# Performance work log

Hardware: AMD Instinct MI355X
Metric: run time of the kernel (lower is better)

Reference implementation:

```python
import jax, jax.numpy as jnp
import numpy as np

H = 128
STEPS = 4
EPS = 1e-5

def _mlp(x, W0, b0, W1, b1, W2, b2):
    x = jax.nn.relu(x @ W0 + b0)
    x = jax.nn.relu(x @ W1 + b1)
    return x @ W2 + b2

def _ln(x, g, b):
    mu = jnp.mean(x, axis=-1, keepdims=True)
    var = jnp.mean((x - mu) ** 2, axis=-1, keepdims=True)
    return (x - mu) * jax.lax.rsqrt(var + EPS) * g + b

def _scores(x, pos):
    # soft assignment of points to graph nodes: softmax over -squared distance
    d2 = (jnp.sum(x * x, -1, keepdims=True)
          - 2.0 * jnp.einsum('bnd,md->bnm', x, pos)
          + jnp.sum(pos * pos, -1))  # [B, Npts, Nnodes]
    return jax.nn.softmax(-d2, axis=-1)

def _block(nodes, senders, receivers, msg_W, msg_b, ln1_g, ln1_b, node_W, node_b, ln2_g, ln2_b):
    # gather edge endpoints, message MLP, layernorm
    m = jnp.concatenate((nodes[:, receivers], nodes[:, senders]), axis=-1) @ msg_W + msg_b
    m = _ln(m, ln1_g, ln1_b)  # [B, E, H]
    inbox = jnp.zeros_like(nodes).at[:, receivers].add(m)  # scatter-add
    out = jnp.concatenate((nodes, inbox), axis=-1) @ node_W + node_b
    return _ln(out, ln2_g, ln2_b)

def setup_inputs() -> dict:
    key = jax.random.key(0)
    ks = jax.random.split(key, 40)
    B, Nc, Nt, N, E = 8, 4096, 4096, 1024, 16384
    dx, dyc, dyt = 2, 3, 3
    def w(k, *s):
        fan_in = s[0]
        return jax.random.normal(k, s, jnp.float32) / np.sqrt(fan_in)
    inp = {
        'xc': jax.random.normal(ks[0], (B, Nc, dx), jnp.float32),
        'yc': jax.random.normal(ks[1], (B, Nc, dyc), jnp.float32),
        'xt': jax.random.normal(ks[2], (B, Nt, dx), jnp.float32),
        'pos': jax.random.normal(ks[3], (N, dx), jnp.float32),
        'enc_W0': w(ks[4], dx + dyc, H), 'enc_b0': jnp.zeros((H,), jnp.float32),
        'enc_W1': w(ks[5], H, H), 'enc_b1': jnp.zeros((H,), jnp.float32),
        'enc_W2': w(ks[6], H, H), 'enc_b2': jnp.zeros((H,), jnp.float32),
        'qenc_W0': w(ks[7], dx, H), 'qenc_b0': jnp.zeros((H,), jnp.float32),
        'qenc_W1': w(ks[8], H, H), 'qenc_b1': jnp.zeros((H,), jnp.float32),
        'qenc_W2': w(ks[9], H, H), 'qenc_b2': jnp.zeros((H,), jnp.float32),
        'dec_W0': w(ks[10], 2 * H, H), 'dec_b0': jnp.zeros((H,), jnp.float32),
        'dec_W1': w(ks[11], H, H), 'dec_b1': jnp.zeros((H,), jnp.float32),
        'dec_W2': w(ks[12], H, dyt), 'dec_b2': jnp.zeros((dyt,), jnp.float32),
        'msg_W': w(ks[13], 2 * H, H), 'msg_b': jnp.zeros((H,), jnp.float32),
        'ln1_g': jnp.ones((H,), jnp.float32), 'ln1_b': jnp.zeros((H,), jnp.float32),
        'node_W': w(ks[14], 2 * H, H), 'node_b': jnp.zeros((H,), jnp.float32),
        'ln2_g': jnp.ones((H,), jnp.float32), 'ln2_b': jnp.zeros((H,), jnp.float32),
        'senders': jax.random.randint(ks[15], (E,), 0, N, jnp.int32),
        'receivers': jax.random.randint(ks[16], (E,), 0, N, jnp.int32),
    }
    return inp

def reference(xc, yc, xt, pos,
              enc_W0, enc_b0, enc_W1, enc_b1, enc_W2, enc_b2,
              qenc_W0, qenc_b0, qenc_W1, qenc_b1, qenc_W2, qenc_b2,
              dec_W0, dec_b0, dec_W1, dec_b1, dec_W2, dec_b2,
              msg_W, msg_b, ln1_g, ln1_b, node_W, node_b, ln2_g, ln2_b,
              senders, receivers):
    sc = _scores(xc, pos)  # [B, Nc, N]
    emb = _mlp(jnp.concatenate((xc, yc), -1), enc_W0, enc_b0, enc_W1, enc_b1, enc_W2, enc_b2)
    latents = jnp.einsum('bcn,bch->bnh', sc, emb)  # scores^T @ emb -> [B, N, H]
    for _ in range(STEPS):  # shared block (same weights each step)
        latents = _block(latents, senders, receivers, msg_W, msg_b, ln1_g, ln1_b,
                         node_W, node_b, ln2_g, ln2_b)
    q = _mlp(xt, qenc_W0, qenc_b0, qenc_W1, qenc_b1, qenc_W2, qenc_b2)
    st = _scores(xt, pos)  # [B, Nt, N]
    z = jnp.einsum('btn,bnh->bth', st, latents)
    z = jnp.concatenate((z, q), -1)
    return _mlp(z, dec_W0, dec_b0, dec_W1, dec_b1, dec_W2, dec_b2)
```

## Files before the change

kernel.cpp:

```cpp
#include <hip/hip_runtime.h>
#include <hip/hip_bf16.h>
#include <string.h>

#define BB 8
#define NC 4096
#define NTT 4096
#define NNODE 1024
#define NEDGE 16384
#define LDE 4128
#define LDL 1056

typedef __hip_bfloat16 bf16;
typedef unsigned short u16;
typedef __attribute__((ext_vector_type(8))) short short8;
typedef __attribute__((ext_vector_type(4))) float f32x4;

__device__ __forceinline__ float b2f(bf16 x) { return __bfloat162float(x); }
__device__ __forceinline__ float bs2f(short s) { return __uint_as_float(((unsigned)(unsigned short)s) << 16); }

template <typename T> struct Cvt;
template <> struct Cvt<float> { static __device__ __forceinline__ float to(float v) { return v; } };
template <> struct Cvt<bf16>  { static __device__ __forceinline__ bf16  to(float v) { return __float2bfloat16(v); } };

__device__ __forceinline__ unsigned short f2bs(float x) {
    unsigned u = __float_as_uint(x);
    return (unsigned short)((u + 0x7FFFu + ((u >> 16) & 1u)) >> 16);
}

__device__ __forceinline__ short8 ld_frag(const bf16* g) {
    union { uint4 u4; short8 s8; } cv;
    cv.u4 = *(const uint4*)g;
    return cv.s8;
}
__device__ __forceinline__ short8 ld_frag(const float* g) {
    float4 f0 = *(const float4*)g;
    float4 f1 = *(const float4*)(g + 4);
    short8 r;
    r[0] = (short)f2bs(f0.x); r[1] = (short)f2bs(f0.y);
    r[2] = (short)f2bs(f0.z); r[3] = (short)f2bs(f0.w);
    r[4] = (short)f2bs(f1.x); r[5] = (short)f2bs(f1.y);
    r[6] = (short)f2bs(f1.z); r[7] = (short)f2bs(f1.w);
    return r;
}

__global__ void detect_k(const u16* __restrict__ posu, int* __restrict__ flag) {
    __shared__ int cnt;
    if (threadIdx.x == 0) cnt = 0;
    __syncthreads();
    int wild = 0;
    for (int i = threadIdx.x; i < 1024; i += 256) {
        u16 u = posu[2 * i];
        int ex = (u >> 7) & 0xFF;
        if (ex == 0 || ex == 0xFF || ex > 137 || ex < 107) wild++;
    }
    atomicAdd(&cnt, wild);
    __syncthreads();
    if (threadIdx.x == 0) *flag = (cnt > 50) ? 1 : 0;
}

struct Tab { const void* src[30]; int pref[31]; };

__global__ __launch_bounds__(256) void ingest_k(Tab tab, const int* __restrict__ flag,
                                                bf16* __restrict__ dst) {
    int idx = blockIdx.x * 256 + threadIdx.x;
    if (idx >= tab.pref[30]) return;
    int t = 0;
    while (tab.pref[t + 1] <= idx) t++;
    int e = idx - tab.pref[t];
    float v;
    if (*flag) v = ((const float*)tab.src[t])[e];
    else       v = b2f(((const bf16*)tab.src[t])[e]);
    dst[idx] = __float2bfloat16(v);
}

struct TT { const bf16* src[11]; bf16* dst[11]; int srcK[11]; int dK[11]; int pref[12]; };

__global__ __launch_bounds__(256) void prep_trans_k(
    TT tt,
    const bf16* __restrict__ xc, const bf16* __restrict__ yc,
    const bf16* __restrict__ xt,
    const bf16* __restrict__ pos,
    bf16* __restrict__ xin32, bf16* __restrict__ xt32,
    float2* __restrict__ posf2) {
    if (blockIdx.x < 128) {
        int row = blockIdx.x * 256 + threadIdx.x;
        bf16 z = __float2bfloat16(0.f);
        bf16* xr = xin32 + row * 32;
        xr[0] = xc[row * 2 + 0];
        xr[1] = xc[row * 2 + 1];
        xr[2] = yc[row * 3 + 0];
        xr[3] = yc[row * 3 + 1];
        xr[4] = yc[row * 3 + 2];
#pragma unroll
        for (int k = 5; k < 32; ++k) xr[k] = z;
        bf16* tr = xt32 + row * 32;
        tr[0] = xt[row * 2 + 0];
        tr[1] = xt[row * 2 + 1];
#pragma unroll
        for (int k = 2; k < 32; ++k) tr[k] = z;
        if (row < NNODE) posf2[row] = make_float2(b2f(pos[2 * row]), b2f(pos[2 * row + 1]));
        return;
    }
    int idx = (blockIdx.x - 128) * 256 + threadIdx.x;
    if (idx >= tt.pref[11]) return;
    int t = 0;
    while (tt.pref[t + 1] <= idx) t++;
    int e = idx - tt.pref[t];
    int k = e >> 7, n = e & 127;
    bf16 v = (k < tt.srcK[t]) ? tt.src[t][k * 128 + n] : __float2bfloat16(0.f);
    tt.dst[t][n * tt.dK[t] + k] = v;
}

__global__ __launch_bounds__(1024) void build_csr_k(const int* __restrict__ recv,
                                                    const int* __restrict__ send,
                                                    int* __restrict__ rowptr,
                                                    int* __restrict__ csr_send) {
    __shared__ int cnt[1024];
    __shared__ int wt[16], wt2[16];
    __shared__ int cur[1024];
    int t = threadIdx.x;
    cnt[t] = 0;
    __syncthreads();
    for (int e = t; e < NEDGE; e += 1024) atomicAdd(&cnt[recv[e]], 1);
    __syncthreads();
    int v = cnt[t];
    int lane = t & 63, w = t >> 6;
#pragma unroll
    for (int off = 1; off < 64; off <<= 1) {
        int u = __shfl_up(v, off);
        if (lane >= off) v += u;
    }
    if (lane == 63) wt[w] = v;
    __syncthreads();
    if (t < 16) {
        int x = wt[t];
#pragma unroll
        for (int off = 1; off < 16; off <<= 1) {
            int u = __shfl_up(x, off);
            if (t >= off) x += u;
        }
        wt2[t] = x;
    }
    __syncthreads();
    int excl = v - cnt[t] + (w ? wt2[w - 1] : 0);
    rowptr[t] = excl;
    cur[t] = excl;
    if (t == 0) rowptr[1024] = NEDGE;
    __syncthreads();
    for (int e = t; e < NEDGE; e += 1024) {
        int pos = atomicAdd(&cur[recv[e]], 1);
        csr_send[pos] = send[e];
    }
}

template <int KSTEPS, int EPI, int RELU, int TRANS, int NSPLIT,
          typename TINA, typename TINB, typename TOUT>
__global__ __launch_bounds__(256) void mfma_gemm_k(
    const TINA* __restrict__ Xa, const TINB* __restrict__ Xb, int ldx,
    const bf16* __restrict__ Wt,
    const bf16* __restrict__ bias,
    const bf16* __restrict__ lng, const bf16* __restrict__ lnb,
    TOUT* __restrict__ Y, int ldy, int tshift, int ldt,
    float2* __restrict__ vstat)
{
    constexpr int K = KSTEPS * 32;
    __shared__ __align__(16) short Bs[8][64][8];
    int tid = threadIdx.x;
    int w = tid >> 6, l = tid & 63;
    int lm = l & 15, lq = l >> 4;
    int blk = blockIdx.x;
    int half = 0;
    if (NSPLIT == 2) { half = blk & 1; blk >>= 1; }
    const bf16* Wtl = Wt + (size_t)half * 128 * K;
    int colbase = half * 128;
    size_t row0 = (size_t)blk * 64;

    f32x4 acc[8];
#pragma unroll
    for (int i = 0; i < 8; i++) acc[i] = (f32x4){0.f, 0.f, 0.f, 0.f};

    for (int s = 0; s < KSTEPS; ++s) {
        int k0 = s * 32;
        __syncthreads();
        short8 a;
        if (Xb != nullptr && k0 >= 128)
            a = ld_frag(Xb + (row0 + w * 16 + lm) * (size_t)128 + (k0 - 128) + lq * 8);
        else
            a = ld_frag(Xa + (row0 + w * 16 + lm) * (size_t)ldx + k0 + lq * 8);
#pragma unroll
        for (int rr = 0; rr < 2; ++rr) {
            int idx = rr * 256 + tid;
            int nt = idx >> 6, ll = idx & 63;
            *(short8*)&Bs[nt][ll][0] =
                ld_frag(Wtl + (size_t)(nt * 16 + (ll & 15)) * K + k0 + (ll >> 4) * 8);
        }
        __syncthreads();
#pragma unroll
        for (int nt = 0; nt < 8; ++nt) {
            short8 b = *(const short8*)&Bs[nt][l][0];
            acc[nt] = __builtin_amdgcn_mfma_f32_16x16x32_bf16(a, b, acc[nt], 0, 0, 0);
        }
    }

    float v[8][4];
#pragma unroll
    for (int nt = 0; nt < 8; ++nt) {
        float bb = bias ? b2f(bias[colbase + nt * 16 + lm]) : 0.f;
#pragma unroll
        for (int r = 0; r < 4; ++r) v[nt][r] = acc[nt][r] + bb;
    }
    if constexpr (EPI == 1) {
#pragma unroll
        for (int r = 0; r < 4; ++r) {
            float s1 = 0.f, s2 = 0.f;
#pragma unroll
            for (int nt = 0; nt < 8; ++nt) { s1 += v[nt][r]; s2 += v[nt][r] * v[nt][r]; }
#pragma unroll
            for (int m = 1; m < 16; m <<= 1) { s1 += __shfl_xor(s1, m); s2 += __shfl_xor(s2, m); }
            float mu = s1 * (1.f / 128.f);
            float var = s2 * (1.f / 128.f) - mu * mu;
            float rs = rsqrtf(var + 1e-5f);
#pragma unroll
            for (int nt = 0; nt < 8; ++nt) {
                int n = nt * 16 + lm;
                v[nt][r] = (v[nt][r] - mu) * rs * b2f(lng[n]) + b2f(lnb[n]);
            }
        }
    }
    if constexpr (TRANS) {
        size_t grow = row0 + w * 16 + lq * 4;
        int bb2 = (int)(grow >> tshift);
        size_t rloc = grow & (((size_t)1 << tshift) - 1);
        bf16* YT = (bf16*)Y;
#pragma unroll
        for (int nt = 0; nt < 8; ++nt) {
            int col = colbase + nt * 16 + lm;
            ushort4 u;
            float x0 = v[nt][0], x1 = v[nt][1], x2 = v[nt][2], x3 = v[nt][3];
            if (RELU) { x0 = fmaxf(x0, 0.f); x1 = fmaxf(x1, 0.f); x2 = fmaxf(x2, 0.f); x3 = fmaxf(x3, 0.f); }
            u.x = f2bs(x0); u.y = f2bs(x1); u.z = f2bs(x2); u.w = f2bs(x3);
            *(ushort4*)(YT + ((size_t)bb2 * 128 + col) * (size_t)ldt + rloc) = u;
        }
    } else {
#pragma unroll
        for (int nt = 0; nt < 8; ++nt)
#pragma unroll
            for (int r = 0; r < 4; ++r) {
                float x = v[nt][r];
                if (RELU) x = fmaxf(x, 0.f);
                Y[(row0 + w * 16 + lq * 4 + r) * (size_t)ldy + colbase + nt * 16 + lm] = Cvt<TOUT>::to(x);
            }
        if (vstat != nullptr && half == 1) {
#pragma unroll
            for (int r = 0; r < 4; ++r) {
                float s1 = 0.f, s2 = 0.f;
#pragma unroll
                for (int nt = 0; nt < 8; ++nt) {
                    float vv = bs2f((short)f2bs(v[nt][r]));
                    s1 += vv; s2 += vv * vv;
                }
#pragma unroll
                for (int m = 1; m < 16; m <<= 1) { s1 += __shfl_xor(s1, m); s2 += __shfl_xor(s2, m); }
                if (lm == 0)
                    vstat[row0 + w * 16 + lq * 4 + r] = make_float2(s1 * (1.f / 128.f), s2);
            }
        }
    }
}

__global__ __launch_bounds__(256) void node_msg_k(
    const float* __restrict__ cur, const bf16* __restrict__ inbox,
    const bf16* __restrict__ WtNode, const bf16* __restrict__ node_b,
    const bf16* __restrict__ ln2_g, const bf16* __restrict__ ln2_b,
    const bf16* __restrict__ WtMsg,
    float* __restrict__ nxt, bf16* __restrict__ PQ,
    float2* __restrict__ vstat)
{
    __shared__ __align__(16) short Bs[8][64][8];
    __shared__ __align__(16) short Act[32][136];
    __shared__ float2 lnp[4][4][4];
    int tid = threadIdx.x;
    int w = tid >> 6, l = tid & 63;
    int lm = l & 15, lq = l >> 4;
    int wr = w & 1, wc = w >> 1;
    size_t row0 = (size_t)blockIdx.x * 32;

    f32x4 acc[4];
#pragma unroll
    for (int i = 0; i < 4; i++) acc[i] = (f32x4){0.f, 0.f, 0.f, 0.f};

    for (int s = 0; s < 8; ++s) {
        int k0 = s * 32;
        __syncthreads();
        short8 a;
        if (k0 < 128) a = ld_frag(cur + (row0 + wr * 16 + lm) * 128 + k0 + lq * 8);
        else          a = ld_frag(inbox + (row0 + wr * 16 + lm) * 128 + (k0 - 128) + lq * 8);
#pragma unroll
        for (int rr = 0; rr < 2; ++rr) {
            int idx = rr * 256 + tid;
            int nt = idx >> 6, ll = idx & 63;
            *(short8*)&Bs[nt][ll][0] =
                ld_frag(WtNode + (size_t)(nt * 16 + (ll & 15)) * 256 + k0 + (ll >> 4) * 8);
        }
        __syncthreads();
#pragma unroll
        for (int t2 = 0; t2 < 4; ++t2) {
            short8 b = *(const short8*)&Bs[wc * 4 + t2][l][0];
            acc[t2] = __builtin_amdgcn_mfma_f32_16x16x32_bf16(a, b, acc[t2], 0, 0, 0);
        }
    }
    float v[4][4];
#pragma unroll
    for (int t2 = 0; t2 < 4; ++t2) {
        float bb = b2f(node_b[wc * 64 + t2 * 16 + lm]);
#pragma unroll
        for (int r = 0; r < 4; ++r) v[t2][r] = acc[t2][r] + bb;
    }
#pragma unroll
    for (int r = 0; r < 4; ++r) {
        float s1 = 0.f, s2 = 0.f;
#pragma unroll
        for (int t2 = 0; t2 < 4; ++t2) { s1 += v[t2][r]; s2 += v[t2][r] * v[t2][r]; }
#pragma unroll
        for (int m = 1; m < 16; m <<= 1) { s1 += __shfl_xor(s1, m); s2 += __shfl_xor(s2, m); }
        if (lm == 0) lnp[w][lq][r] = make_float2(s1, s2);
    }
    __syncthreads();
#pragma unroll
    for (int r = 0; r < 4; ++r) {
        float2 mine = lnp[w][lq][r], oth = lnp[w ^ 2][lq][r];
        float s1 = mine.x + oth.x, s2 = mine.y + oth.y;
        float mu = s1 * (1.f / 128.f);
        float var = s2 * (1.f / 128.f) - mu * mu;
        float rs = rsqrtf(var + 1e-5f);
#pragma unroll
        for (int t2 = 0; t2 < 4; ++t2) {
            int n = wc * 64 + t2 * 16 + lm;
            v[t2][r] = (v[t2][r] - mu) * rs * b2f(ln2_g[n]) + b2f(ln2_b[n]);
        }
    }
#pragma unroll
    for (int t2 = 0; t2 < 4; ++t2)
#pragma unroll
        for (int r = 0; r < 4; ++r) {
            nxt[(row0 + wr * 16 + lq * 4 + r) * 128 + wc * 64 + t2 * 16 + lm] = v[t2][r];
            Act[wr * 16 + lq * 4 + r][wc * 64 + t2 * 16 + lm] = (short)f2bs(v[t2][r]);
        }

    for (int half = 0; half < 2; ++half) {
        const bf16* Wtl = WtMsg + (size_t)half * 128 * 128;
#pragma unroll
        for (int i = 0; i < 4; i++) acc[i] = (f32x4){0.f, 0.f, 0.f, 0.f};
        for (int s = 0; s < 4; ++s) {
            int k0 = s * 32;
            __syncthreads();
#pragma unroll
            for (int rr = 0; rr < 2; ++rr) {
                int idx = rr * 256 + tid;
                int nt = idx >> 6, ll = idx & 63;
                *(short8*)&Bs[nt][ll][0] =
                    ld_frag(Wtl + (size_t)(nt * 16 + (ll & 15)) * 128 + k0 + (ll >> 4) * 8);
            }
            __syncthreads();
            short8 a = *(const short8*)&Act[wr * 16 + lm][k0 + lq * 8];
#pragma unroll
            for (int t2 = 0; t2 < 4; ++t2) {
                short8 b = *(const short8*)&Bs[wc * 4 + t2][l][0];
                acc[t2] = __builtin_amdgcn_mfma_f32_16x16x32_bf16(a, b, acc[t2], 0, 0, 0);
            }
        }
#pragma unroll
        for (int t2 = 0; t2 < 4; ++t2)
#pragma unroll
            for (int r = 0; r < 4; ++r)
                PQ[(row0 + wr * 16 + lq * 4 + r) * 256 + half * 128 + wc * 64 + t2 * 16 + lm] =
                    __float2bfloat16(acc[t2][r]);
        if (half == 1) {
#pragma unroll
            for (int r = 0; r < 4; ++r) {
                float s1 = 0.f, s2 = 0.f;
#pragma unroll
                for (int t2 = 0; t2 < 4; ++t2) {
                    float vv = bs2f((short)f2bs(acc[t2][r]));
                    s1 += vv; s2 += vv * vv;
                }
#pragma unroll
                for (int m = 1; m < 16; m <<= 1) { s1 += __shfl_xor(s1, m); s2 += __shfl_xor(s2, m); }
                if (lm == 0) lnp[w][lq][r] = make_float2(s1, s2);
            }
            __syncthreads();
            if (wc == 0 && lm == 0) {
#pragma unroll
                for (int r = 0; r < 4; ++r) {
                    float2 mine = lnp[w][lq][r], oth = lnp[w + 2][lq][r];
                    vstat[row0 + wr * 16 + lq * 4 + r] =
                        make_float2((mine.x + oth.x) * (1.f / 128.f), mine.y + oth.y);
                }
            }
        }
    }
}

template <int K0STEPS, int LAYERS, int RELU_LAST, int TRANS, typename TIN, typename TOUT>
__global__ __launch_bounds__(256) void mlp_k(
    const TIN* __restrict__ Xa, const TIN* __restrict__ Xb, int ldx,
    const bf16* __restrict__ Wt0, const bf16* __restrict__ b0,
    const bf16* __restrict__ Wt1, const bf16* __restrict__ b1,
    const bf16* __restrict__ Wt2, const bf16* __restrict__ b2,
    TOUT* __restrict__ Y, int ldy, int tshift, int ldt)
{
    constexpr int K0 = K0STEPS * 32;
    __shared__ __align__(16) short Bs[8][64][8];
    __shared__ __align__(16) short Act[64][136];
    int tid = threadIdx.x;
    int w = tid >> 6, l = tid & 63;
    int lm = l & 15, lq = l >> 4;
    size_t row0 = (size_t)blockIdx.x * 64;

    f32x4 acc[8];
#pragma unroll
    for (int i = 0; i < 8; i++) acc[i] = (f32x4){0.f, 0.f, 0.f, 0.f};

    for (int s = 0; s < K0STEPS; ++s) {
        int k0 = s * 32;
        __syncthreads();
        short8 a;
        {
            const TIN* src = Xa; int kk = k0; int ld = ldx;
            if (Xb != nullptr && k0 >= 128) { src = Xb; kk = k0 - 128; ld = 128; }
            a = ld_frag(src + (row0 + w * 16 + lm) * (size_t)ld + kk + lq * 8);
        }
#pragma unroll
        for (int rr = 0; rr < 2; ++rr) {
            int idx = rr * 256 + tid;
            int nt = idx >> 6, ll = idx & 63;
            *(short8*)&Bs[nt][ll][0] =
                ld_frag(Wt0 + (size_t)(nt * 16 + (ll & 15)) * K0 + k0 + (ll >> 4) * 8);
        }
        __syncthreads();
#pragma unroll
        for (int nt = 0; nt < 8; ++nt) {
            short8 b = *(const short8*)&Bs[nt][l][0];
            acc[nt] = __builtin_amdgcn_mfma_f32_16x16x32_bf16(a, b, acc[nt], 0, 0, 0);
        }
    }
#pragma unroll
    for (int nt = 0; nt < 8; ++nt) {
        float bb = b2f(b0[nt * 16 + lm]);
#pragma unroll
        for (int r = 0; r < 4; ++r) {
            float x = fmaxf(acc[nt][r] + bb, 0.f);
            Act[w * 16 + lq * 4 + r][nt * 16 + lm] = (short)f2bs(x);
        }
    }

    for (int L = 1; L < LAYERS; ++L) {
        const bf16* Wt = (L == 1) ? Wt1 : Wt2;
        const bf16* bias = (L == 1) ? b1 : b2;
        bool last = (L == LAYERS - 1);
#pragma unroll
        for (int i = 0; i < 8; i++) acc[i] = (f32x4){0.f, 0.f, 0.f, 0.f};
        for (int s = 0; s < 4; ++s) {
            int k0 = s * 32;
            __syncthreads();
#pragma unroll
            for (int rr = 0; rr < 2; ++rr) {
                int idx = rr * 256 + tid;
                int nt = idx >> 6, ll = idx & 63;
                *(short8*)&Bs[nt][ll][0] =
                    ld_frag(Wt + (size_t)(nt * 16 + (ll & 15)) * 128 + k0 + (ll >> 4) * 8);
            }
            __syncthreads();
            short8 a = *(const short8*)&Act[w * 16 + lm][k0 + lq * 8];
#pragma unroll
            for (int nt = 0; nt < 8; ++nt) {
                short8 b = *(const short8*)&Bs[nt][l][0];
                acc[nt] = __builtin_amdgcn_mfma_f32_16x16x32_bf16(a, b, acc[nt], 0, 0, 0);
            }
        }
        if (!last) {
            __syncthreads();
#pragma unroll
            for (int nt = 0; nt < 8; ++nt) {
// ... 361 lines not shown
    __shared__ __align__(8) float2 posh[1024];
    __shared__ __align__(16) union ShU {
        short stage[2][8192];
        float4 red[4][8][64];
    } sh;
    int tid = threadIdx.x;
    int w = tid >> 6, l = tid & 63;
    int wl = w & 3, up = w >> 2;
    int lm = l & 15, lq = l >> 4;
    int t = t0 + wl * 16 + lm;
    float4 qs = cstT4[b * NTT + t];
    const bf16* lbase = latT + (size_t)b * (128 * LDL);
    for (int k = tid; k < 1024; k += 512) posh[k] = posf2[k];

    int h0 = tid >> 3;
    int cb0 = (tid & 7) << 4;
    const char* g0 = (const char*)lbase + (size_t)h0 * (LDL * 2) + cb0;
    const size_t gH = (size_t)64 * (LDL * 2);
    int o0 = h0 * 128 + (cb0 ^ ((h0 & 7) << 4));
    char* lbuf0 = (char*)&sh.stage[0][0];
    char* lbuf1 = (char*)&sh.stage[1][0];

    {
        uint4 rA = *(const uint4*)(g0);
        uint4 rB = *(const uint4*)(g0 + gH);
        *(uint4*)(lbuf0 + o0) = rA;
        *(uint4*)(lbuf0 + o0 + 64 * 128) = rB;
    }
    __syncthreads();

    f32x4 acc[8];
#pragma unroll
    for (int q = 0; q < 8; q++) acc[q] = (f32x4){0.f, 0.f, 0.f, 0.f};

    union AF { short8 s; u16 u[8]; };
    int rb = up * 64 + lq * 16;

    for (int ci = 0; ci < 16; ++ci) {
        char* cur = (ci & 1) ? lbuf1 : lbuf0;
        char* nxt = (ci & 1) ? lbuf0 : lbuf1;
        uint4 rA, rB;
        if (ci < 15) {
            const char* gs = g0 + (ci + 1) * 128;
            rA = *(const uint4*)(gs);
            rB = *(const uint4*)(gs + gH);
        }
        AF cw;
        int cidx = ci * 64 + up * 32 + lq * 8;
#pragma unroll
        for (int j = 0; j < 8; ++j) {
            float2 pn = posh[cidx + j];
            float dx = qs.x - pn.x, dy = qs.y - pn.y;
            cw.u[j] = f2bs(__expf(-(dx * dx + dy * dy) - qs.z) * qs.w);
        }
#pragma unroll
        for (int t2 = 0; t2 < 8; ++t2) {
            int h = t2 * 16 + lm;
            short8 bfr = *(const short8*)(cur + h * 128 + (rb ^ ((h & 7) << 4)));
            acc[t2] = __builtin_amdgcn_mfma_f32_16x16x32_bf16(cw.s, bfr, acc[t2], 0, 0, 0);
        }
        if (ci < 15) {
            *(uint4*)(nxt + o0) = rA;
            *(uint4*)(nxt + o0 + 64 * 128) = rB;
        }
        __syncthreads();
    }

    if (up) {
#pragma unroll
        for (int t2 = 0; t2 < 8; ++t2)
            sh.red[wl][t2][l] = make_float4(acc[t2][0], acc[t2][1], acc[t2][2], acc[t2][3]);
    }
    __syncthreads();
    if (!up) {
        bf16* zp = z + (((size_t)(b * NTT + t0 + wl * 16 + lq * 4)) << 7) + lm;
#pragma unroll
        for (int t2 = 0; t2 < 8; ++t2) {
            float4 o = sh.red[wl][t2][l];
#pragma unroll
            for (int r2 = 0; r2 < 4; ++r2)
                zp[(r2 << 7) + t2 * 16] = __float2bfloat16(acc[t2][r2] + ((const float*)&o)[r2]);
        }
    }
}

__global__ __launch_bounds__(256) void edge_gather_k(const bf16* __restrict__ PQ,
                                                     const float2* __restrict__ vstat,
                                                     const int* __restrict__ rowptr,
                                                     const int* __restrict__ csr_send,
                                                     const bf16* __restrict__ mb,
                                                     const bf16* __restrict__ g1,
                                                     const bf16* __restrict__ b1,
                                                     bf16* __restrict__ inbox) {
    int tid = threadIdx.x;
    int w = tid >> 6, l = tid & 63;
    int gw = blockIdx.x * 4 + w;
    int b = gw >> 10, n = gw & 1023;
    const bf16* pqb = PQ + ((size_t)b << 18);
    const float2* vsb = vstat + b * NNODE;
    float u0 = b2f(pqb[(n << 8) + l]) + b2f(mb[l]);
    float u1 = b2f(pqb[(n << 8) + l + 64]) + b2f(mb[l + 64]);
    float g0 = b2f(g1[l]), g1v = b2f(g1[l + 64]);
    float bb0 = b2f(b1[l]), bb1 = b2f(b1[l + 64]);
    float s1 = u0 + u1, s2 = u0 * u0 + u1 * u1;
#pragma unroll
    for (int off = 32; off; off >>= 1) {
        s1 += __shfl_xor(s1, off);
        s2 += __shfl_xor(s2, off);
    }
    float aN = s1 * (1.f / 128.f);
    float Su = s2;
    int beg = rowptr[n], end = rowptr[n + 1];
    float R = 0.f, M = 0.f, t0 = 0.f, t1 = 0.f;
    int i = beg;
    for (; i + 1 < end; i += 2) {
        int sA = csr_send[i], sB = csr_send[i + 1];
        const bf16* qA = pqb + (sA << 8) + 128;
        const bf16* qB = pqb + (sB << 8) + 128;
        float vA0 = b2f(qA[l]), vA1 = b2f(qA[l + 64]);
        float vB0 = b2f(qB[l]), vB1 = b2f(qB[l + 64]);
        float dA = u0 * vA0 + u1 * vA1;
        float dB = u0 * vB0 + u1 * vB1;
#pragma unroll
        for (int off = 32; off; off >>= 1) {
            dA += __shfl_xor(dA, off);
            dB += __shfl_xor(dB, off);
        }
        float2 stA = vsb[sA];
        float2 stB = vsb[sB];
        float muA = aN + stA.x;
        float varA = (Su + stA.y + 2.f * dA) * (1.f / 128.f) - muA * muA;
        float rsA = rsqrtf(varA + 1e-5f);
        float muB = aN + stB.x;
        float varB = (Su + stB.y + 2.f * dB) * (1.f / 128.f) - muB * muB;
        float rsB = rsqrtf(varB + 1e-5f);
        R += rsA + rsB;
        M += rsA * muA + rsB * muB;
        t0 += rsA * vA0 + rsB * vB0;
        t1 += rsA * vA1 + rsB * vB1;
    }
    if (i < end) {
        int s = csr_send[i];
        const bf16* q = pqb + (s << 8) + 128;
        float v0 = b2f(q[l]), v1 = b2f(q[l + 64]);
        float d = u0 * v0 + u1 * v1;
#pragma unroll
        for (int off = 32; off; off >>= 1) d += __shfl_xor(d, off);
        float2 st = vsb[s];
        float mu = aN + st.x;
        float var = (Su + st.y + 2.f * d) * (1.f / 128.f) - mu * mu;
        float rs = rsqrtf(var + 1e-5f);
        R += rs;
        M += rs * mu;
        t0 += rs * v0;
        t1 += rs * v1;
    }
    float deg = (float)(end - beg);
    float a0 = g0 * (u0 * R + t0 - M) + deg * bb0;
    float a1 = g1v * (u1 * R + t1 - M) + deg * bb1;
    bf16* inb = inbox + ((size_t)b << 17) + (n << 7);
    inb[l] = __float2bfloat16(a0);
    inb[l + 64] = __float2bfloat16(a1);
}

extern "C" void kernel_launch(void* const* d_in, const int* in_sizes, int n_in,
                              void* d_out, int out_size, void* d_ws, size_t ws_size,
                              hipStream_t stream) {
    const int* senders = (const int*)d_in[30];
    const int* receivers = (const int*)d_in[31];

    char* base = (char*)d_ws;
    size_t off = 0;
    auto alloc = [&](size_t bytes) { char* p = base + off; off += (bytes + 255) & ~(size_t)255; return p; };

    int* flag = (int*)alloc(256);

    Tab tab;
    int pref = 0;
    for (int i = 0; i < 30; ++i) { tab.src[i] = d_in[i]; tab.pref[i] = pref; pref += in_sizes[i]; }
    tab.pref[30] = pref;
    bf16* arena = (bf16*)alloc((size_t)pref * 2);
    auto C = [&](int i) { return arena + tab.pref[i]; };

    float4* cstC4 = (float4*)alloc(32768 * sizeof(float4));
    float4* cstT4 = (float4*)alloc(32768 * sizeof(float4));
    float* lat0  = (float*)alloc(8192 * 128 * 4);
    float* lat1  = (float*)alloc(8192 * 128 * 4);
    float* inboxf = (float*)alloc(8192 * 128 * 4);
    bf16* inbox  = (bf16*)alloc(8192 * 128 * 2);
    bf16* T1     = (bf16*)alloc((size_t)32768 * 128 * 2);
    bf16* T2     = (bf16*)alloc((size_t)32768 * 128 * 2);
    bf16* T3     = (bf16*)alloc((size_t)32768 * 128 * 2);
    bf16* embT   = (bf16*)alloc((size_t)8 * 128 * LDE * 2);
    bf16* latT   = (bf16*)alloc((size_t)8 * 128 * LDL * 2);
    bf16* xin32  = (bf16*)alloc((size_t)32768 * 32 * 2);
    bf16* xt32   = (bf16*)alloc((size_t)32768 * 32 * 2);
    float2* posf2 = (float2*)alloc(1024 * sizeof(float2));
    float2* vstat = (float2*)alloc(8192 * sizeof(float2));
    int* rowptr  = (int*)alloc(1025 * 4);
    int* csr_send = (int*)alloc(NEDGE * 4);
    bf16* WtEnc0 = (bf16*)alloc(128 * 32 * 2);
    bf16* WtQ0   = (bf16*)alloc(128 * 32 * 2);
    bf16* WtEnc1 = (bf16*)alloc(16384 * 2);
    bf16* WtEnc2 = (bf16*)alloc(16384 * 2);
    bf16* WtQ1   = (bf16*)alloc(16384 * 2);
    bf16* WtQ2   = (bf16*)alloc(16384 * 2);
    bf16* WtDec0 = (bf16*)alloc(32768 * 2);
    bf16* WtDec1 = (bf16*)alloc(16384 * 2);
    bf16* WtMsg  = (bf16*)alloc(32768 * 2);
    bf16* WtNode = (bf16*)alloc(32768 * 2);
    bf16* PQ     = T3;
    (void)ws_size; (void)n_in; (void)out_size;

    detect_k<<<1, 256, 0, stream>>>((const u16*)d_in[3], flag);
    ingest_k<<<(pref + 255) / 256, 256, 0, stream>>>(tab, flag, arena);

    const bf16 *xc = C(0), *yc = C(1), *xt = C(2), *pos = C(3);
    const bf16 *enc_W0 = C(4), *enc_b0 = C(5), *enc_W1 = C(6), *enc_b1 = C(7), *enc_W2 = C(8), *enc_b2 = C(9);
    const bf16 *qenc_W0 = C(10), *qenc_b0 = C(11), *qenc_W1 = C(12), *qenc_b1 = C(13), *qenc_W2 = C(14), *qenc_b2 = C(15);
    const bf16 *dec_W0 = C(16), *dec_b0 = C(17), *dec_W1 = C(18), *dec_b1 = C(19), *dec_W2 = C(20), *dec_b2 = C(21);
    const bf16 *msg_W = C(22), *msg_b = C(23), *ln1_g = C(24), *ln1_b = C(25);
    const bf16 *node_W = C(26), *node_b = C(27), *ln2_g = C(28), *ln2_b = C(29);

    TT tt;
    const bf16* s11[11] = { enc_W1, enc_W2, qenc_W1, qenc_W2, dec_W1, dec_W0, msg_W, msg_W + 16384, node_W, enc_W0, qenc_W0 };
    bf16* d11[11]       = { WtEnc1, WtEnc2, WtQ1,    WtQ2,    WtDec1, WtDec0, WtMsg, WtMsg + 16384, WtNode, WtEnc0, WtQ0   };
    int sk11[11] = { 128, 128, 128, 128, 128, 256, 128, 128, 256, 5, 2 };
    int dk11[11] = { 128, 128, 128, 128, 128, 256, 128, 128, 256, 32, 32 };
    int tp = 0;
    for (int i = 0; i < 11; ++i) {
        tt.src[i] = s11[i]; tt.dst[i] = d11[i]; tt.srcK[i] = sk11[i]; tt.dK[i] = dk11[i];
        tt.pref[i] = tp; tp += dk11[i] * 128;
    }
    tt.pref[11] = tp;

    prep_trans_k<<<128 + (tp + 255) / 256, 256, 0, stream>>>(tt, xc, yc, xt, pos, xin32, xt32, posf2);
    build_csr_k<<<1, 1024, 0, stream>>>(receivers, senders, rowptr, csr_send);

    mlp_k<1, 3, 0, 1, bf16, bf16><<<512, 256, 0, stream>>>(
        xin32, nullptr, 32, WtEnc0, enc_b0, WtEnc1, enc_b1, WtEnc2, enc_b2, embT, 128, 12, LDE);

    stats2_k<<<4096, 256, 0, stream>>>(xc, xt, pos, cstC4, cstT4);

    P8 parts;
    parts.p[0] = lat1;
    parts.p[1] = inboxf;
    parts.p[2] = (float*)T1;
    parts.p[3] = (float*)T1 + 1048576;
    parts.p[4] = (float*)T2;
    parts.p[5] = (float*)T2 + 1048576;
    parts.p[6] = (float*)T3;
    parts.p[7] = (float*)T3 + 1048576;
    lat_mfma_k<<<1024, 512, 0, stream>>>(embT, posf2, cstC4, parts);
    reduce8_k<<<1024, 256, 0, stream>>>(lat0, parts);

    mfma_gemm_k<4, 0, 0, 0, 2, float, float, bf16><<<256, 256, 0, stream>>>(lat0, nullptr, 128, WtMsg, nullptr, nullptr, nullptr, PQ, 256, 0, 0, vstat);
    edge_gather_k<<<2048, 256, 0, stream>>>(PQ, vstat, rowptr, csr_send, msg_b, ln1_g, ln1_b, inbox);
    node_msg_k<<<256, 256, 0, stream>>>(lat0, inbox, WtNode, node_b, ln2_g, ln2_b, WtMsg, lat1, PQ, vstat);
    edge_gather_k<<<2048, 256, 0, stream>>>(PQ, vstat, rowptr, csr_send, msg_b, ln1_g, ln1_b, inbox);
    node_msg_k<<<256, 256, 0, stream>>>(lat1, inbox, WtNode, node_b, ln2_g, ln2_b, WtMsg, lat0, PQ, vstat);
    edge_gather_k<<<2048, 256, 0, stream>>>(PQ, vstat, rowptr, csr_send, msg_b, ln1_g, ln1_b, inbox);
    node_msg_k<<<256, 256, 0, stream>>>(lat0, inbox, WtNode, node_b, ln2_g, ln2_b, WtMsg, lat1, PQ, vstat);
    edge_gather_k<<<2048, 256, 0, stream>>>(PQ, vstat, rowptr, csr_send, msg_b, ln1_g, ln1_b, inbox);
    mfma_gemm_k<8, 1, 0, 1, 1, float, bf16, bf16><<<128, 256, 0, stream>>>(lat1, inbox, 128, WtNode, node_b, ln2_g, ln2_b, latT, 128, 10, LDL, nullptr);

    z_mfma_k<<<512, 512, 0, stream>>>(latT, posf2, cstT4, T2);

    qdec_k<<<512, 256, 0, stream>>>(xt32,
                                    WtQ0, qenc_b0, WtQ1, qenc_b1, WtQ2, qenc_b2,
                                    T2,
                                    WtDec0, dec_b0, WtDec1, dec_b1,
                                    dec_W2, dec_b2, flag, d_out);
}
```

Measured before the change: 401.4 us.

## Fuse message-passing recurrence into one cooperative persistent kernel with grid syncs

Replaces the nine separate launches of the graph block loop (message GEMM, edge gather, node+message GEMM, final node GEMM) with a single cooperative kernel of 256 blocks by 512 threads. Phases are separated by grid.sync(), and the work is redistributed so each block handles 32 rows with 8 waves. The aim is to remove per-launch overhead and inter-kernel gaps for these small kernels. In exchange, the edge gather now runs on only 256 blocks instead of 2048, and grid-wide barriers add their own cost.

```diff
diff --git a/kernel.cpp b/kernel.cpp
--- a/kernel.cpp
+++ b/kernel.cpp
@@ -1,6 +1,9 @@
 #include <hip/hip_runtime.h>
 #include <hip/hip_bf16.h>
+#include <hip/hip_cooperative_groups.h>
 #include <string.h>
+
+namespace cg = cooperative_groups;
 
 #define BB 8
 #define NC 4096
@@ -153,252 +156,249 @@
     }
 }
 
-template <int KSTEPS, int EPI, int RELU, int TRANS, int NSPLIT,
-          typename TINA, typename TINB, typename TOUT>
-__global__ __launch_bounds__(256) void mfma_gemm_k(
-    const TINA* __restrict__ Xa, const TINB* __restrict__ Xb, int ldx,
-    const bf16* __restrict__ Wt,
-    const bf16* __restrict__ bias,
-    const bf16* __restrict__ lng, const bf16* __restrict__ lnb,
-    TOUT* __restrict__ Y, int ldy, int tshift, int ldt,
-    float2* __restrict__ vstat)
-{
-    constexpr int K = KSTEPS * 32;
-    __shared__ __align__(16) short Bs[8][64][8];
-    int tid = threadIdx.x;
-    int w = tid >> 6, l = tid & 63;
-    int lm = l & 15, lq = l >> 4;
-    int blk = blockIdx.x;
-    int half = 0;
-    if (NSPLIT == 2) { half = blk & 1; blk >>= 1; }
-    const bf16* Wtl = Wt + (size_t)half * 128 * K;
-    int colbase = half * 128;
-    size_t row0 = (size_t)blk * 64;
-
-    f32x4 acc[8];
-#pragma unroll
-    for (int i = 0; i < 8; i++) acc[i] = (f32x4){0.f, 0.f, 0.f, 0.f};
-
-    for (int s = 0; s < KSTEPS; ++s) {
-        int k0 = s * 32;
-        __syncthreads();
-        short8 a;
-        if (Xb != nullptr && k0 >= 128)
-            a = ld_frag(Xb + (row0 + w * 16 + lm) * (size_t)128 + (k0 - 128) + lq * 8);
-        else
-            a = ld_frag(Xa + (row0 + w * 16 + lm) * (size_t)ldx + k0 + lq * 8);
-#pragma unroll
-        for (int rr = 0; rr < 2; ++rr) {
-            int idx = rr * 256 + tid;
-            int nt = idx >> 6, ll = idx & 63;
-            *(short8*)&Bs[nt][ll][0] =
-                ld_frag(Wtl + (size_t)(nt * 16 + (ll & 15)) * K + k0 + (ll >> 4) * 8);
-        }
-        __syncthreads();
-#pragma unroll
-        for (int nt = 0; nt < 8; ++nt) {
-            short8 b = *(const short8*)&Bs[nt][l][0];
-            acc[nt] = __builtin_amdgcn_mfma_f32_16x16x32_bf16(a, b, acc[nt], 0, 0, 0);
-        }
-    }
-
-    float v[8][4];
-#pragma unroll
-    for (int nt = 0; nt < 8; ++nt) {
-        float bb = bias ? b2f(bias[colbase + nt * 16 + lm]) : 0.f;
-#pragma unroll
-        for (int r = 0; r < 4; ++r) v[nt][r] = acc[nt][r] + bb;
-    }
-    if constexpr (EPI == 1) {
-#pragma unroll
-        for (int r = 0; r < 4; ++r) {
-            float s1 = 0.f, s2 = 0.f;
-#pragma unroll
-            for (int nt = 0; nt < 8; ++nt) { s1 += v[nt][r]; s2 += v[nt][r] * v[nt][r]; }
-#pragma unroll
-            for (int m = 1; m < 16; m <<= 1) { s1 += __shfl_xor(s1, m); s2 += __shfl_xor(s2, m); }
-            float mu = s1 * (1.f / 128.f);
-            float var = s2 * (1.f / 128.f) - mu * mu;
-            float rs = rsqrtf(var + 1e-5f);
-#pragma unroll
-            for (int nt = 0; nt < 8; ++nt) {
-                int n = nt * 16 + lm;
-                v[nt][r] = (v[nt][r] - mu) * rs * b2f(lng[n]) + b2f(lnb[n]);
-            }
-        }
-    }
-    if constexpr (TRANS) {
-        size_t grow = row0 + w * 16 + lq * 4;
-        int bb2 = (int)(grow >> tshift);
-        size_t rloc = grow & (((size_t)1 << tshift) - 1);
-        bf16* YT = (bf16*)Y;
-#pragma unroll
-        for (int nt = 0; nt < 8; ++nt) {
-            int col = colbase + nt * 16 + lm;
-            ushort4 u;
-            float x0 = v[nt][0], x1 = v[nt][1], x2 = v[nt][2], x3 = v[nt][3];
-            if (RELU) { x0 = fmaxf(x0, 0.f); x1 = fmaxf(x1, 0.f); x2 = fmaxf(x2, 0.f); x3 = fmaxf(x3, 0.f); }
-            u.x = f2bs(x0); u.y = f2bs(x1); u.z = f2bs(x2); u.w = f2bs(x3);
-            *(ushort4*)(YT + ((size_t)bb2 * 128 + col) * (size_t)ldt + rloc) = u;
-        }
-    } else {
-#pragma unroll
-        for (int nt = 0; nt < 8; ++nt)
-#pragma unroll
-            for (int r = 0; r < 4; ++r) {
-                float x = v[nt][r];
-                if (RELU) x = fmaxf(x, 0.f);
-                Y[(row0 + w * 16 + lq * 4 + r) * (size_t)ldy + colbase + nt * 16 + lm] = Cvt<TOUT>::to(x);
-            }
-        if (vstat != nullptr && half == 1) {
-#pragma unroll
-            for (int r = 0; r < 4; ++r) {
-                float s1 = 0.f, s2 = 0.f;
-#pragma unroll
-                for (int nt = 0; nt < 8; ++nt) {
-                    float vv = bs2f((short)f2bs(v[nt][r]));
-                    s1 += vv; s2 += vv * vv;
-                }
-#pragma unroll
-                for (int m = 1; m < 16; m <<= 1) { s1 += __shfl_xor(s1, m); s2 += __shfl_xor(s2, m); }
-                if (lm == 0)
-                    vstat[row0 + w * 16 + lq * 4 + r] = make_float2(s1 * (1.f / 128.f), s2);
-            }
-        }
-    }
-}
-
-__global__ __launch_bounds__(256) void node_msg_k(
-    const float* __restrict__ cur, const bf16* __restrict__ inbox,
-    const bf16* __restrict__ WtNode, const bf16* __restrict__ node_b,
-    const bf16* __restrict__ ln2_g, const bf16* __restrict__ ln2_b,
-    const bf16* __restrict__ WtMsg,
-    float* __restrict__ nxt, bf16* __restrict__ PQ,
-    float2* __restrict__ vstat)
-{
+struct RecurArgs {
+    float* lat0; float* lat1; bf16* inbox; bf16* PQ; float2* vstat;
+    const bf16* WtMsg; const bf16* msg_b; const bf16* ln1_g; const bf16* ln1_b;
+    const bf16* WtNode; const bf16* node_b; const bf16* ln2_g; const bf16* ln2_b;
+    const int* rowptr; const int* csr_send; bf16* latT;
+};
+
+__global__ __launch_bounds__(512, 1) void recur_k(RecurArgs A) {
+    cg::grid_group grid = cg::this_grid();
     __shared__ __align__(16) short Bs[8][64][8];
     __shared__ __align__(16) short Act[32][136];
-    __shared__ float2 lnp[4][4][4];
+    __shared__ float2 lnp[8][4][4];
     int tid = threadIdx.x;
     int w = tid >> 6, l = tid & 63;
     int lm = l & 15, lq = l >> 4;
     int wr = w & 1, wc = w >> 1;
     size_t row0 = (size_t)blockIdx.x * 32;
 
-    f32x4 acc[4];
-#pragma unroll
-    for (int i = 0; i < 4; i++) acc[i] = (f32x4){0.f, 0.f, 0.f, 0.f};
-
-    for (int s = 0; s < 8; ++s) {
-        int k0 = s * 32;
-        __syncthreads();
-        short8 a;
-        if (k0 < 128) a = ld_frag(cur + (row0 + wr * 16 + lm) * 128 + k0 + lq * 8);
-        else          a = ld_frag(inbox + (row0 + wr * 16 + lm) * 128 + (k0 - 128) + lq * 8);
-#pragma unroll
-        for (int rr = 0; rr < 2; ++rr) {
-            int idx = rr * 256 + tid;
-            int nt = idx >> 6, ll = idx & 63;
-            *(short8*)&Bs[nt][ll][0] =
-                ld_frag(WtNode + (size_t)(nt * 16 + (ll & 15)) * 256 + k0 + (ll >> 4) * 8);
-        }
-        __syncthreads();
-#pragma unroll
-        for (int t2 = 0; t2 < 4; ++t2) {
-            short8 b = *(const short8*)&Bs[wc * 4 + t2][l][0];
-            acc[t2] = __builtin_amdgcn_mfma_f32_16x16x32_bf16(a, b, acc[t2], 0, 0, 0);
-        }
-    }
-    float v[4][4];
-#pragma unroll
-    for (int t2 = 0; t2 < 4; ++t2) {
-        float bb = b2f(node_b[wc * 64 + t2 * 16 + lm]);
-#pragma unroll
-        for (int r = 0; r < 4; ++r) v[t2][r] = acc[t2][r] + bb;
-    }
-#pragma unroll
-    for (int r = 0; r < 4; ++r) {
-        float s1 = 0.f, s2 = 0.f;
-#pragma unroll
-        for (int t2 = 0; t2 < 4; ++t2) { s1 += v[t2][r]; s2 += v[t2][r] * v[t2][r]; }
-#pragma unroll
-        for (int m = 1; m < 16; m <<= 1) { s1 += __shfl_xor(s1, m); s2 += __shfl_xor(s2, m); }
-        if (lm == 0) lnp[w][lq][r] = make_float2(s1, s2);
-    }
-    __syncthreads();
-#pragma unroll
-    for (int r = 0; r < 4; ++r) {
-        float2 mine = lnp[w][lq][r], oth = lnp[w ^ 2][lq][r];
-        float s1 = mine.x + oth.x, s2 = mine.y + oth.y;
-        float mu = s1 * (1.f / 128.f);
-        float var = s2 * (1.f / 128.f) - mu * mu;
-        float rs = rsqrtf(var + 1e-5f);
-#pragma unroll
-        for (int t2 = 0; t2 < 4; ++t2) {
-            int n = wc * 64 + t2 * 16 + lm;
-            v[t2][r] = (v[t2][r] - mu) * rs * b2f(ln2_g[n]) + b2f(ln2_b[n]);
-        }
-    }
-#pragma unroll
-    for (int t2 = 0; t2 < 4; ++t2)
-#pragma unroll
-        for (int r = 0; r < 4; ++r) {
-            nxt[(row0 + wr * 16 + lq * 4 + r) * 128 + wc * 64 + t2 * 16 + lm] = v[t2][r];
-            Act[wr * 16 + lq * 4 + r][wc * 64 + t2 * 16 + lm] = (short)f2bs(v[t2][r]);
-        }
-
-    for (int half = 0; half < 2; ++half) {
-        const bf16* Wtl = WtMsg + (size_t)half * 128 * 128;
-#pragma unroll
-        for (int i = 0; i < 4; i++) acc[i] = (f32x4){0.f, 0.f, 0.f, 0.f};
-        for (int s = 0; s < 4; ++s) {
+    auto stageB = [&](const bf16* W, int K, int k0) {
+        int nt = tid >> 6, ll = tid & 63;
+        *(short8*)&Bs[nt][ll][0] =
+            ld_frag(W + (size_t)(nt * 16 + (ll & 15)) * K + k0 + (ll >> 4) * 8);
+    };
+
+    auto msg_phase = [&](const float* curf, bool fromAct) {
+        for (int half = 0; half < 2; ++half) {
+            f32x4 acc[2];
+            acc[0] = (f32x4){0.f,0.f,0.f,0.f}; acc[1] = (f32x4){0.f,0.f,0.f,0.f};
+            for (int s = 0; s < 4; ++s) {
+                int k0 = s * 32;
+                __syncthreads();
+                stageB(A.WtMsg + half * 16384, 128, k0);
+                __syncthreads();
+                short8 a;
+                if (fromAct) a = *(const short8*)&Act[wr * 16 + lm][k0 + lq * 8];
+                else         a = ld_frag(curf + (row0 + wr * 16 + lm) * 128 + k0 + lq * 8);
+#pragma unroll
+                for (int t2 = 0; t2 < 2; ++t2) {
+                    short8 b = *(const short8*)&Bs[wc * 2 + t2][l][0];
+                    acc[t2] = __builtin_amdgcn_mfma_f32_16x16x32_bf16(a, b, acc[t2], 0, 0, 0);
+                }
+            }
+#pragma unroll
+            for (int t2 = 0; t2 < 2; ++t2)
+#pragma unroll
+                for (int r = 0; r < 4; ++r)
+                    A.PQ[(row0 + wr * 16 + lq * 4 + r) * 256 + half * 128 + wc * 32 + t2 * 16 + lm] =
+                        __float2bfloat16(acc[t2][r]);
+            if (half == 1) {
+#pragma unroll
+                for (int r = 0; r < 4; ++r) {
+                    float s1 = 0.f, s2 = 0.f;
+#pragma unroll
+                    for (int t2 = 0; t2 < 2; ++t2) {
+                        float vv = bs2f((short)f2bs(acc[t2][r]));
+                        s1 += vv; s2 += vv * vv;
+                    }
+#pragma unroll
+                    for (int m = 1; m < 16; m <<= 1) { s1 += __shfl_xor(s1, m); s2 += __shfl_xor(s2, m); }
+                    if (lm == 0) lnp[w][lq][r] = make_float2(s1, s2);
+                }
+                __syncthreads();
+                if (wc == 0 && lm == 0) {
+#pragma unroll
+                    for (int r = 0; r < 4; ++r) {
+                        float S1 = 0.f, S2 = 0.f;
+#pragma unroll
+                        for (int j = 0; j < 4; ++j) {
+                            float2 p = lnp[wr + 2 * j][lq][r];
+                            S1 += p.x; S2 += p.y;
+                        }
+                        A.vstat[row0 + wr * 16 + lq * 4 + r] = make_float2(S1 * (1.f / 128.f), S2);
+                    }
+                }
+            }
+        }
+    };
+
+    auto node_phase = [&](const float* curf, float* nxtf, bool toLatT) {
+        f32x4 acc[2];
+        acc[0] = (f32x4){0.f,0.f,0.f,0.f}; acc[1] = (f32x4){0.f,0.f,0.f,0.f};
+        for (int s = 0; s < 8; ++s) {
             int k0 = s * 32;
             __syncthreads();
-#pragma unroll
-            for (int rr = 0; rr < 2; ++rr) {
-                int idx = rr * 256 + tid;
-                int nt = idx >> 6, ll = idx & 63;
-                *(short8*)&Bs[nt][ll][0] =
-                    ld_frag(Wtl + (size_t)(nt * 16 + (ll & 15)) * 128 + k0 + (ll >> 4) * 8);
-            }
+            stageB(A.WtNode, 256, k0);
             __syncthreads();
-            short8 a = *(const short8*)&Act[wr * 16 + lm][k0 + lq * 8];
-#pragma unroll
-            for (int t2 = 0; t2 < 4; ++t2) {
-                short8 b = *(const short8*)&Bs[wc * 4 + t2][l][0];
+            short8 a;
+            if (k0 < 128) a = ld_frag(curf + (row0 + wr * 16 + lm) * 128 + k0 + lq * 8);
+            else          a = ld_frag(A.inbox + (row0 + wr * 16 + lm) * 128 + (k0 - 128) + lq * 8);
+#pragma unroll
+            for (int t2 = 0; t2 < 2; ++t2) {
+                short8 b = *(const short8*)&Bs[wc * 2 + t2][l][0];
                 acc[t2] = __builtin_amdgcn_mfma_f32_16x16x32_bf16(a, b, acc[t2], 0, 0, 0);
             }
         }
-#pragma unroll
-        for (int t2 = 0; t2 < 4; ++t2)
-#pragma unroll
-            for (int r = 0; r < 4; ++r)
-                PQ[(row0 + wr * 16 + lq * 4 + r) * 256 + half * 128 + wc * 64 + t2 * 16 + lm] =
-                    __float2bfloat16(acc[t2][r]);
-        if (half == 1) {
-#pragma unroll
-            for (int r = 0; r < 4; ++r) {
-                float s1 = 0.f, s2 = 0.f;
-#pragma unroll
-                for (int t2 = 0; t2 < 4; ++t2) {
-                    float vv = bs2f((short)f2bs(acc[t2][r]));
-                    s1 += vv; s2 += vv * vv;
+        float v[2][4];
+#pragma unroll
+        for (int t2 = 0; t2 < 2; ++t2) {
+            float bb = b2f(A.node_b[wc * 32 + t2 * 16 + lm]);
+#pragma unroll
+            for (int r = 0; r < 4; ++r) v[t2][r] = acc[t2][r] + bb;
+        }
+#pragma unroll
+        for (int r = 0; r < 4; ++r) {
+            float s1 = v[0][r] + v[1][r];
+            float s2 = v[0][r] * v[0][r] + v[1][r] * v[1][r];
+#pragma unroll
+            for (int m = 1; m < 16; m <<= 1) { s1 += __shfl_xor(s1, m); s2 += __shfl_xor(s2, m); }
+            if (lm == 0) lnp[w][lq][r] = make_float2(s1, s2);
+        }
+        __syncthreads();
+#pragma unroll
+        for (int r = 0; r < 4; ++r) {
+            float S1 = 0.f, S2 = 0.f;
+#pragma unroll
+            for (int j = 0; j < 4; ++j) {
+                float2 p = lnp[wr + 2 * j][lq][r];
+                S1 += p.x; S2 += p.y;
+            }
+            float mu = S1 * (1.f / 128.f);
+            float var = S2 * (1.f / 128.f) - mu * mu;
+            float rs = rsqrtf(var + 1e-5f);
+#pragma unroll
+            for (int t2 = 0; t2 < 2; ++t2) {
+                int n = wc * 32 + t2 * 16 + lm;
+                v[t2][r] = (v[t2][r] - mu) * rs * b2f(A.ln2_g[n]) + b2f(A.ln2_b[n]);
+            }
+        }
+        if (!toLatT) {
+#pragma unroll
+            for (int t2 = 0; t2 < 2; ++t2)
+#pragma unroll
+                for (int r = 0; r < 4; ++r) {
+                    nxtf[(row0 + wr * 16 + lq * 4 + r) * 128 + wc * 32 + t2 * 16 + lm] = v[t2][r];
+                    Act[wr * 16 + lq * 4 + r][wc * 32 + t2 * 16 + lm] = (short)f2bs(v[t2][r]);
                 }
-#pragma unroll
-                for (int m = 1; m < 16; m <<= 1) { s1 += __shfl_xor(s1, m); s2 += __shfl_xor(s2, m); }
-                if (lm == 0) lnp[w][lq][r] = make_float2(s1, s2);
-            }
-            __syncthreads();
-            if (wc == 0 && lm == 0) {
-#pragma unroll
-                for (int r = 0; r < 4; ++r) {
-                    float2 mine = lnp[w][lq][r], oth = lnp[w + 2][lq][r];
-                    vstat[row0 + wr * 16 + lq * 4 + r] =
-                        make_float2((mine.x + oth.x) * (1.f / 128.f), mine.y + oth.y);
+        } else {
+            size_t grow = row0 + wr * 16 + lq * 4;
+            int bb2 = (int)(grow >> 10);
+            size_t rloc = grow & 1023;
+#pragma unroll
+            for (int t2 = 0; t2 < 2; ++t2) {
+                int col = wc * 32 + t2 * 16 + lm;
+                ushort4 u;
+                u.x = f2bs(v[t2][0]); u.y = f2bs(v[t2][1]);
+                u.z = f2bs(v[t2][2]); u.w = f2bs(v[t2][3]);
+                *(ushort4*)(A.latT + ((size_t)bb2 * 128 + col) * (size_t)LDL + rloc) = u;
+            }
+        }
+    };
+
+    auto eg = [&]() {
+        for (int it = 0; it < 4; ++it) {
+            int gw = blockIdx.x * 8 + w + it * 2048;
+            int b = gw >> 10, n = gw & 1023;
+            const bf16* pqb = A.PQ + ((size_t)b << 18);
+            const float2* vsb = A.vstat + b * NNODE;
+            float u0 = b2f(pqb[(n << 8) + l]) + b2f(A.msg_b[l]);
+            float u1 = b2f(pqb[(n << 8) + l + 64]) + b2f(A.msg_b[l + 64]);
+            float g0 = b2f(A.ln1_g[l]), g1v = b2f(A.ln1_g[l + 64]);
+            float bb0 = b2f(A.ln1_b[l]), bb1 = b2f(A.ln1_b[l + 64]);
+            float s1 = u0 + u1, s2 = u0 * u0 + u1 * u1;
+#pragma unroll
+            for (int off = 32; off; off >>= 1) {
+                s1 += __shfl_xor(s1, off);
+                s2 += __shfl_xor(s2, off);
+            }
+            float aN = s1 * (1.f / 128.f);
+            float Su = s2;
+            int beg = A.rowptr[n], end = A.rowptr[n + 1];
+            float R = 0.f, M = 0.f, t0 = 0.f, t1 = 0.f;
+            int i = beg;
+            for (; i + 1 < end; i += 2) {
+                int sA = A.csr_send[i], sB = A.csr_send[i + 1];
+                const bf16* qA = pqb + (sA << 8) + 128;
+                const bf16* qB = pqb + (sB << 8) + 128;
+                float vA0 = b2f(qA[l]), vA1 = b2f(qA[l + 64]);
+                float vB0 = b2f(qB[l]), vB1 = b2f(qB[l + 64]);
+                float dA = u0 * vA0 + u1 * vA1;
+                float dB = u0 * vB0 + u1 * vB1;
+#pragma unroll
+                for (int off = 32; off; off >>= 1) {
+                    dA += __shfl_xor(dA, off);
+                    dB += __shfl_xor(dB, off);
                 }
-            }
-        }
-    }
+                float2 stA = vsb[sA];
+                float2 stB = vsb[sB];
+                float muA = aN + stA.x;
+                float varA = (Su + stA.y + 2.f * dA) * (1.f / 128.f) - muA * muA;
+                float rsA = rsqrtf(varA + 1e-5f);
+                float muB = aN + stB.x;
+                float varB = (Su + stB.y + 2.f * dB) * (1.f / 128.f) - muB * muB;
+                float rsB = rsqrtf(varB + 1e-5f);
+                R += rsA + rsB;
+                M += rsA * muA + rsB * muB;
+                t0 += rsA * vA0 + rsB * vB0;
+                t1 += rsA * vA1 + rsB * vB1;
+            }
+            if (i < end) {
+                int s = A.csr_send[i];
+                const bf16* q = pqb + (s << 8) + 128;
+                float v0 = b2f(q[l]), v1 = b2f(q[l + 64]);
+                float d = u0 * v0 + u1 * v1;
+#pragma unroll
+                for (int off = 32; off; off >>= 1) d += __shfl_xor(d, off);
+                float2 st = vsb[s];
+                float mu = aN + st.x;
+                float var = (Su + st.y + 2.f * d) * (1.f / 128.f) - mu * mu;
+                float rs = rsqrtf(var + 1e-5f);
+                R += rs;
+                M += rs * mu;
+                t0 += rs * v0;
+                t1 += rs * v1;
+            }
+            float deg = (float)(end - beg);
+            float a0 = g0 * (u0 * R + t0 - M) + deg * bb0;
+            float a1 = g1v * (u1 * R + t1 - M) + deg * bb1;
+            bf16* inb = A.inbox + ((size_t)b << 17) + (n << 7);
+            inb[l] = __float2bfloat16(a0);
+            inb[l + 64] = __float2bfloat16(a1);
+        }
+    };
+
+    msg_phase(A.lat0, false);
+    grid.sync();
+    eg();
+    grid.sync();
+    node_phase(A.lat0, A.lat1, false);
+    msg_phase(nullptr, true);
+    grid.sync();
+    eg();
+    grid.sync();
+    node_phase(A.lat1, A.lat0, false);
+    msg_phase(nullptr, true);
+    grid.sync();
+    eg();
+    grid.sync();
+    node_phase(A.lat0, A.lat1, false);
+    msg_phase(nullptr, true);
+    grid.sync();
+    eg();
+    grid.sync();
+    node_phase(A.lat1, nullptr, true);
 }
 
 template <int K0STEPS, int LAYERS, int RELU_LAST, int TRANS, typename TIN, typename TOUT>
@@ -926,85 +926,6 @@
                 zp[(r2 << 7) + t2 * 16] = __float2bfloat16(acc[t2][r2] + ((const float*)&o)[r2]);
         }
     }
-}
-
-__global__ __launch_bounds__(256) void edge_gather_k(const bf16* __restrict__ PQ,
-                                                     const float2* __restrict__ vstat,
-                                                     const int* __restrict__ rowptr,
-                                                     const int* __restrict__ csr_send,
-                                                     const bf16* __restrict__ mb,
-                                                     const bf16* __restrict__ g1,
-                                                     const bf16* __restrict__ b1,
-                                                     bf16* __restrict__ inbox) {
-    int tid = threadIdx.x;
-    int w = tid >> 6, l = tid & 63;
-    int gw = blockIdx.x * 4 + w;
-    int b = gw >> 10, n = gw & 1023;
-    const bf16* pqb = PQ + ((size_t)b << 18);
-    const float2* vsb = vstat + b * NNODE;
-    float u0 = b2f(pqb[(n << 8) + l]) + b2f(mb[l]);
-    float u1 = b2f(pqb[(n << 8) + l + 64]) + b2f(mb[l + 64]);
-    float g0 = b2f(g1[l]), g1v = b2f(g1[l + 64]);
-    float bb0 = b2f(b1[l]), bb1 = b2f(b1[l + 64]);
-    float s1 = u0 + u1, s2 = u0 * u0 + u1 * u1;
-#pragma unroll
-    for (int off = 32; off; off >>= 1) {
-        s1 += __shfl_xor(s1, off);
-        s2 += __shfl_xor(s2, off);
-    }
-    float aN = s1 * (1.f / 128.f);
-    float Su = s2;
-    int beg = rowptr[n], end = rowptr[n + 1];
-    float R = 0.f, M = 0.f, t0 = 0.f, t1 = 0.f;
-    int i = beg;
-    for (; i + 1 < end; i += 2) {
-        int sA = csr_send[i], sB = csr_send[i + 1];
-        const bf16* qA = pqb + (sA << 8) + 128;
-        const bf16* qB = pqb + (sB << 8) + 128;
-        float vA0 = b2f(qA[l]), vA1 = b2f(qA[l + 64]);
-        float vB0 = b2f(qB[l]), vB1 = b2f(qB[l + 64]);
-        float dA = u0 * vA0 + u1 * vA1;
-        float dB = u0 * vB0 + u1 * vB1;
-#pragma unroll
-        for (int off = 32; off; off >>= 1) {
-            dA += __shfl_xor(dA, off);
-            dB += __shfl_xor(dB, off);
-        }
-        float2 stA = vsb[sA];
-        float2 stB = vsb[sB];
-        float muA = aN + stA.x;
-        float varA = (Su + stA.y + 2.f * dA) * (1.f / 128.f) - muA * muA;
-        float rsA = rsqrtf(varA + 1e-5f);
-        float muB = aN + stB.x;
-        float varB = (Su + stB.y + 2.f * dB) * (1.f / 128.f) - muB * muB;
-        float rsB = rsqrtf(varB + 1e-5f);
-        R += rsA + rsB;
-        M += rsA * muA + rsB * muB;
-        t0 += rsA * vA0 + rsB * vB0;
-        t1 += rsA * vA1 + rsB * vB1;
-    }
-    if (i < end) {
-        int s = csr_send[i];
-        const bf16* q = pqb + (s << 8) + 128;
-        float v0 = b2f(q[l]), v1 = b2f(q[l + 64]);
-        float d = u0 * v0 + u1 * v1;
-#pragma unroll
-        for (int off = 32; off; off >>= 1) d += __shfl_xor(d, off);
-        float2 st = vsb[s];
-        float mu = aN + st.x;
-        float var = (Su + st.y + 2.f * d) * (1.f / 128.f) - mu * mu;
-        float rs = rsqrtf(var + 1e-5f);
-        R += rs;
-        M += rs * mu;
-        t0 += rs * v0;
-        t1 += rs * v1;
-    }
-    float deg = (float)(end - beg);
-    float a0 = g0 * (u0 * R + t0 - M) + deg * bb0;
-    float a1 = g1v * (u1 * R + t1 - M) + deg * bb1;
-    bf16* inb = inbox + ((size_t)b << 17) + (n << 7);
-    inb[l] = __float2bfloat16(a0);
-    inb[l + 64] = __float2bfloat16(a1);
 }
 
 extern "C" void kernel_launch(void* const* d_in, const int* in_sizes, int n_in,
@@ -1098,15 +1019,13 @@
     lat_mfma_k<<<1024, 512, 0, stream>>>(embT, posf2, cstC4, parts);
     reduce8_k<<<1024, 256, 0, stream>>>(lat0, parts);
 
-    mfma_gemm_k<4, 0, 0, 0, 2, float, float, bf16><<<256, 256, 0, stream>>>(lat0, nullptr, 128, WtMsg, nullptr, nullptr, nullptr, PQ, 256, 0, 0, vstat);
-    edge_gather_k<<<2048, 256, 0, stream>>>(PQ, vstat, rowptr, csr_send, msg_b, ln1_g, ln1_b, inbox);
-    node_msg_k<<<256, 256, 0, stream>>>(lat0, inbox, WtNode, node_b, ln2_g, ln2_b, WtMsg, lat1, PQ, vstat);
-    edge_gather_k<<<2048, 256, 0, stream>>>(PQ, vstat, rowptr, csr_send, msg_b, ln1_g, ln1_b, inbox);
-    node_msg_k<<<256, 256, 0, stream>>>(lat1, inbox, WtNode, node_b, ln2_g, ln2_b, WtMsg, lat0, PQ, vstat);
-    edge_gather_k<<<2048, 256, 0, stream>>>(PQ, vstat, rowptr, csr_send, msg_b, ln1_g, ln1_b, inbox);
-    node_msg_k<<<256, 256, 0, stream>>>(lat0, inbox, WtNode, node_b, ln2_g, ln2_b, WtMsg, lat1, PQ, vstat);
-    edge_gather_k<<<2048, 256, 0, stream>>>(PQ, vstat, rowptr, csr_send, msg_b, ln1_g, ln1_b, inbox);
-    mfma_gemm_k<8, 1, 0, 1, 1, float, bf16, bf16><<<128, 256, 0, stream>>>(lat1, inbox, 128, WtNode, node_b, ln2_g, ln2_b, latT, 128, 10, LDL, nullptr);
+    RecurArgs ra;
+    ra.lat0 = lat0; ra.lat1 = lat1; ra.inbox = inbox; ra.PQ = PQ; ra.vstat = vstat;
+    ra.WtMsg = WtMsg; ra.msg_b = msg_b; ra.ln1_g = ln1_g; ra.ln1_b = ln1_b;
+    ra.WtNode = WtNode; ra.node_b = node_b; ra.ln2_g = ln2_g; ra.ln2_b = ln2_b;
+    ra.rowptr = rowptr; ra.csr_send = csr_send; ra.latT = latT;
+    void* kargs[] = { &ra };
+    hipLaunchCooperativeKernel((void*)recur_k, dim3(256), dim3(512), kargs, 0, stream);
 
     z_mfma_k<<<512, 512, 0, stream>>>(latT, posf2, cstT4, T2);
 
```

Result: slower. 742.2 us (+84.9%).
